# Optimization experiments

Hardware: AMD Instinct MI355X
Metric: run time of the kernel (lower is better)

The kernel has to match this reference:

```python
import jax, jax.numpy as jnp
import numpy as np

jax.config.update("jax_enable_x64", True)

P = 2013265921        # NTT-friendly prime (15 * 2^27 + 1), stand-in for BLS12-381 Fr
G_ROOT = 31           # primitive root of P
LOG_N = 21
N = 1 << LOG_N


def _bit_reverse_perm(n):
    logn = n.bit_length() - 1
    idx = np.arange(n, dtype=np.int64)
    rev = np.zeros(n, dtype=np.int64)
    for b in range(logn):
        rev = (rev << 1) | ((idx >> b) & 1)
    return rev


def _pow_arr(base, exps, mod):
    # vectorized modular exponentiation over numpy int64 exponents (host-side, trace-time)
    res = np.ones_like(exps)
    b = np.int64(base % mod)
    e = exps.copy()
    while e.max() > 0:
        res = np.where(e & 1, (res * b) % mod, res)
        b = (b * b) % mod
        e >>= 1
    return res


_REV = _bit_reverse_perm(N)


def intt(x):
    """Inverse NTT over Z_P, radix-2 DIT with bit-reversal. x: [N] int64 in [0,P)."""
    root = pow(G_ROOT, (P - 1) // N, P)
    iroot = pow(root, P - 2, P)
    x = x[_REV]
    length = 2
    while length <= N:
        half = length // 2
        wlen = pow(iroot, N // length, P)
        tw = jnp.asarray(_pow_arr(wlen, np.arange(half, dtype=np.int64), P))  # [half]
        x = x.reshape(-1, length)
        even, odd = x[:, :half], x[:, half:]
        t = (odd * tw) % P                       # products < 2^62, exact in int64
        x = jnp.concatenate([(even + t) % P, (even - t) % P], axis=1).reshape(-1)
        length *= 2
    n_inv = pow(N, P - 2, P)
    return (x * n_inv) % P


def compress4(a, b, c, d, z):
    """zkp.compress: a + z*b + z^2*c + z^3*d  (mod P). z is a Python int challenge."""
    z1 = z % P
    z2 = (z1 * z1) % P
    z3 = (z2 * z1) % P
    return (a + (b * z1) % P + (c * z2) % P + (d * z3) % P) % P


def commit(poly, bases):
    """KZG commitment proxy: MSM reduced to a scalar-weighted sum of SRS bases."""
    scal = poly.astype(jnp.float32) * np.float32(1.0 / P)  # normalize field elems
    return jnp.einsum('n,nc->c', scal, bases)              # [3]


def reference(w_l, w_r, w_o, w_4, table1, table2, table3, table4,
              q_lookup, powers_of_g, zeta):
    # Round 1: wire polynomials via INTT + commitments via MSM
    w_l_poly = intt(w_l)
    w_r_poly = intt(w_r)
    w_o_poly = intt(w_o)
    w_4_poly = intt(w_4)

    # Lookup: compress tables with zeta, build query table f, split sorted multiset
    t_comp = compress4(table1, table2, table3, table4, zeta)
    table_poly = intt(t_comp)
    w_comp = compress4(w_l, w_r, w_o, w_4, zeta)
    f_comp = jnp.where(q_lookup != 0, w_comp, t_comp)      # compute_query_table
    f_poly = intt(f_comp)

    s = jnp.sort(jnp.concatenate([t_comp, f_comp]))        # combine_split
    h_1, h_2 = s[0::2], s[1::2]
    h_1_poly = intt(h_1)
    h_2_poly = intt(h_2)

    polys = jnp.stack([w_l_poly, w_r_poly, w_o_poly, w_4_poly,
                       table_poly, f_poly, h_1_poly, h_2_poly])  # [8, N]
    commits = jnp.stack([commit(p, powers_of_g) for p in polys])  # [8, 3]
    return commits, polys


def setup_inputs() -> dict:
    key = jax.random.key(0)
    ks = jax.random.split(key, 11)
    fe = lambda k: jax.random.randint(k, (N,), 0, P, dtype=jnp.int64)
    return {
        'w_l': fe(ks[0]), 'w_r': fe(ks[1]), 'w_o': fe(ks[2]), 'w_4': fe(ks[3]),
        'table1': fe(ks[4]), 'table2': fe(ks[5]), 'table3': fe(ks[6]), 'table4': fe(ks[7]),
        'q_lookup': jax.random.randint(ks[8], (N,), 0, 2, dtype=jnp.int64),
        'powers_of_g': jax.random.normal(ks[9], (N, 3), dtype=jnp.float32),
        'zeta': 987654321,
    }
```

## Files before the change

kernel.cpp:

```cpp
#include <hip/hip_runtime.h>
#include <stdint.h>

#define PRIME 2013265921u
#define LOGN 21
#define NN (1u << LOGN)
#define REG 73728u

constexpr uint32_t cpow(uint64_t b, uint64_t e) {
    uint64_t r = 1;
    b %= PRIME;
    while (e) {
        if (e & 1ull) r = r * b % PRIME;
        b = b * b % PRIME;
        e >>= 1;
    }
    return (uint32_t)r;
}
constexpr uint32_t cpinv() {
    uint32_t inv = 1;
    for (int i = 0; i < 6; i++) inv *= 2u - PRIME * inv;
    return inv;
}
constexpr uint32_t NPRIME   = (uint32_t)(0u - cpinv());
constexpr uint32_t RMODP    = (uint32_t)((1ull << 32) % PRIME);
constexpr uint32_t ROOT     = cpow(31u, (PRIME - 1) / NN);
constexpr uint32_t IROOT    = cpow(ROOT, PRIME - 2);
constexpr uint32_t NINV     = cpow(NN, PRIME - 2);
constexpr uint32_t NINV_M   = (uint32_t)((((uint64_t)NINV) << 32) % PRIME);

__device__ __forceinline__ uint32_t addmod(uint32_t a, uint32_t b) {
    uint32_t s = a + b; return (s >= PRIME) ? s - PRIME : s;
}
__device__ __forceinline__ uint32_t submod(uint32_t a, uint32_t b) {
    return (a >= b) ? (a - b) : (a + PRIME - b);
}
__device__ __forceinline__ uint32_t mulmod(uint32_t a, uint32_t b) {
    return (uint32_t)(((uint64_t)a * (uint64_t)b) % PRIME);
}
__device__ __forceinline__ uint32_t montmul(uint32_t a, uint32_t b) {
    uint64_t t = (uint64_t)a * b;
    uint32_t m = (uint32_t)t * NPRIME;
    uint32_t u = (uint32_t)((t + (uint64_t)m * PRIME) >> 32);
    return (u >= PRIME) ? u - PRIME : u;
}
__device__ uint32_t powmod(uint32_t b, uint32_t e) {
    uint32_t r = 1u;
    while (e) {
        if (e & 1u) r = mulmod(r, b);
        b = mulmod(b, b);
        e >>= 1;
    }
    return r;
}
__device__ __forceinline__ uint32_t tomont(uint32_t x) {
    return (uint32_t)((((uint64_t)x) << 32) % PRIME);
}

__global__ void twiddle_all_kernel(uint32_t* __restrict__ WT1, uint32_t* __restrict__ ROWT,
                                   uint32_t* __restrict__ CW) {
    uint32_t i = blockIdx.x * blockDim.x + threadIdx.x;
    if (i < 4096) {
        if (i == 0) WT1[0] = RMODP;
        else {
            uint32_t s = 31u - __clz(i);
            uint32_t j = i ^ (1u << s);
            WT1[i] = tomont(powmod(IROOT, j << (20u - s)));
        }
    }
    if (i < 512) {
        if (i == 0) ROWT[0] = RMODP;
        else {
            uint32_t t = 31u - __clz(i);
            ROWT[i] = tomont(powmod(IROOT, (i - (1u << t)) << (20u - t)));
        }
    }
    if (i < 36864) {
        uint32_t s = i >> 12, j = i & 4095u;
        CW[i] = tomont(powmod(IROOT, j << (8u - s)));
    }
}

__global__ void init_cursor_kernel(unsigned int* __restrict__ ccursor) {
    if (threadIdx.x < 64) ccursor[threadIdx.x] = threadIdx.x * REG;
}

__global__ __launch_bounds__(256) void compress_scatter_kernel(
        const int* __restrict__ wl, const int* __restrict__ wr,
        const int* __restrict__ wo, const int* __restrict__ w4,
        const int* __restrict__ t1, const int* __restrict__ t2,
        const int* __restrict__ t3, const int* __restrict__ t4,
        const int* __restrict__ q,  const int* __restrict__ zp,
        uint32_t* __restrict__ tcomp, uint32_t* __restrict__ fcomp,
        unsigned int* __restrict__ ccursor, uint32_t* __restrict__ barr1) {
    __shared__ uint32_t grp[4096];
    __shared__ unsigned char grpb[4096];
    __shared__ unsigned int cnt[64], pref[64], curs[64], rbase[64];
    uint32_t tid = threadIdx.x;
    uint32_t i0 = blockIdx.x * 2048u + tid * 8u;
    if (tid < 64) cnt[tid] = 0;
    __syncthreads();

    uint32_t z1 = ((uint32_t)zp[0]) % PRIME;
    uint32_t z2 = mulmod(z1, z1);
    uint32_t z3 = mulmod(z2, z1);
    uint32_t tv[8], fv[8];
    #pragma unroll
    for (int h = 0; h < 2; h++) {
        uint32_t ib = i0 + (uint32_t)h * 4u;
        int4 a1 = *reinterpret_cast<const int4*>(&t1[ib]);
        int4 a2 = *reinterpret_cast<const int4*>(&t2[ib]);
        int4 a3 = *reinterpret_cast<const int4*>(&t3[ib]);
        int4 a4 = *reinterpret_cast<const int4*>(&t4[ib]);
        int4 b1 = *reinterpret_cast<const int4*>(&wl[ib]);
        int4 b2 = *reinterpret_cast<const int4*>(&wr[ib]);
        int4 b3 = *reinterpret_cast<const int4*>(&wo[ib]);
        int4 b4 = *reinterpret_cast<const int4*>(&w4[ib]);
        int4 qq = *reinterpret_cast<const int4*>(&q[ib]);
        int av1[4] = {a1.x, a1.y, a1.z, a1.w};
        int av2[4] = {a2.x, a2.y, a2.z, a2.w};
        int av3[4] = {a3.x, a3.y, a3.z, a3.w};
        int av4[4] = {a4.x, a4.y, a4.z, a4.w};
        int bv1[4] = {b1.x, b1.y, b1.z, b1.w};
        int bv2[4] = {b2.x, b2.y, b2.z, b2.w};
        int bv3[4] = {b3.x, b3.y, b3.z, b3.w};
        int bv4[4] = {b4.x, b4.y, b4.z, b4.w};
        int qv[4]  = {qq.x, qq.y, qq.z, qq.w};
        #pragma unroll
        for (int j = 0; j < 4; j++) {
            uint32_t t = addmod(addmod((uint32_t)av1[j], mulmod((uint32_t)av2[j], z1)),
                                addmod(mulmod((uint32_t)av3[j], z2), mulmod((uint32_t)av4[j], z3)));
            uint32_t w = addmod(addmod((uint32_t)bv1[j], mulmod((uint32_t)bv2[j], z1)),
                                addmod(mulmod((uint32_t)bv3[j], z2), mulmod((uint32_t)bv4[j], z3)));
            tv[h * 4 + j] = t;
            fv[h * 4 + j] = (qv[j] != 0) ? w : t;
        }
    }
    *reinterpret_cast<uint4*>(&tcomp[i0])     = make_uint4(tv[0], tv[1], tv[2], tv[3]);
    *reinterpret_cast<uint4*>(&tcomp[i0 + 4]) = make_uint4(tv[4], tv[5], tv[6], tv[7]);
    *reinterpret_cast<uint4*>(&fcomp[i0])     = make_uint4(fv[0], fv[1], fv[2], fv[3]);
    *reinterpret_cast<uint4*>(&fcomp[i0 + 4]) = make_uint4(fv[4], fv[5], fv[6], fv[7]);

    #pragma unroll
    for (int j = 0; j < 8; j++) {
        atomicAdd(&cnt[tv[j] >> 25], 1u);
        atomicAdd(&cnt[fv[j] >> 25], 1u);
    }
    __syncthreads();
    if (tid == 0) {
        unsigned int run = 0;
        for (int b = 0; b < 64; b++) { pref[b] = run; curs[b] = run; run += cnt[b]; }
    }
    __syncthreads();
    if (tid < 64 && cnt[tid]) rbase[tid] = atomicAdd(&ccursor[tid], cnt[tid]);
    #pragma unroll
    for (int j = 0; j < 8; j++) {
        uint32_t v = tv[j];
        uint32_t b = v >> 25;
        unsigned int p = atomicAdd(&curs[b], 1u);
        grp[p] = v; grpb[p] = (unsigned char)b;
    }
    #pragma unroll
    for (int j = 0; j < 8; j++) {
        uint32_t v = fv[j];
        uint32_t b = v >> 25;
        unsigned int p = atomicAdd(&curs[b], 1u);
        grp[p] = v; grpb[p] = (unsigned char)b;
    }
    __syncthreads();
    for (uint32_t l = tid; l < 4096; l += 256) {
        uint32_t b = grpb[l];
        barr1[rbase[b] + (l - pref[b])] = grp[l];
    }
}

#define NBUCK 8192

__global__ __launch_bounds__(256) void fine_hist_kernel(const uint32_t* __restrict__ barr1,
                                                        const unsigned int* __restrict__ ccursor,
                                                        unsigned int* __restrict__ hist) {
    __shared__ unsigned int cnt[128];
    uint32_t tid = threadIdx.x;
    uint32_t reg = blockIdx.y;
    if (tid < 128) cnt[tid] = 0;
    __syncthreads();
    uint32_t lo = reg * REG, hi = ccursor[reg];
    for (uint32_t i = lo + blockIdx.x * 256 + tid; i < hi; i += gridDim.x * 256)
        atomicAdd(&cnt[(barr1[i] >> 18) & 127u], 1u);
    __syncthreads();
    if (tid < 128 && cnt[tid]) atomicAdd(&hist[reg * 128 + tid], cnt[tid]);
}

__global__ void scan_kernel(const unsigned int* __restrict__ hist,
                            unsigned int* __restrict__ basearr, unsigned int* __restrict__ fcursor) {
    __shared__ unsigned int ls[256];
    int t = threadIdx.x;
    unsigned int local[32];
    unsigned int s = 0;
    for (int k = 0; k < 32; k++) { local[k] = hist[t * 32 + k]; s += local[k]; }
    ls[t] = s;
    __syncthreads();
    for (int off = 1; off < 256; off <<= 1) {
        unsigned int v = (t >= off) ? ls[t - off] : 0u;
        __syncthreads();
        ls[t] += v;
        __syncthreads();
    }
    unsigned int run = ls[t] - s;
    for (int k = 0; k < 32; k++) {
        basearr[t * 32 + k] = run;
        fcursor[t * 32 + k] = run;
        run += local[k];
    }
    if (t == 255) basearr[NBUCK] = run;
}

__global__ __launch_bounds__(256) void pass2_kernel(const uint32_t* __restrict__ barr1,
                                                    const unsigned int* __restrict__ ccursor,
                                                    unsigned int* __restrict__ fcursor,
                                                    uint32_t* __restrict__ barr2) {
    __shared__ uint32_t grp[4096];
    __shared__ unsigned char grpb[4096];
    __shared__ unsigned int cnt[128], pref[128], curs[128], rbase[128];
    uint32_t tid = threadIdx.x;
    uint32_t reg = blockIdx.y;
    uint32_t lo = reg * REG, hi = ccursor[reg];
    for (uint32_t start = lo + blockIdx.x * 4096; start < hi; start += gridDim.x * 4096) {
        uint32_t n = min(4096u, hi - start);
        if (tid < 128) cnt[tid] = 0;
        __syncthreads();
        for (uint32_t l = tid; l < n; l += 256)
            atomicAdd(&cnt[(barr1[start + l] >> 18) & 127u], 1u);
        __syncthreads();
        if (tid == 0) {
            unsigned int run = 0;
            for (int b = 0; b < 128; b++) { pref[b] = run; curs[b] = run; run += cnt[b]; }
        }
        __syncthreads();
        if (tid < 128 && cnt[tid]) rbase[tid] = atomicAdd(&fcursor[reg * 128 + tid], cnt[tid]);
        for (uint32_t l = tid; l < n; l += 256) {
            uint32_t v = barr1[start + l];
            uint32_t b = (v >> 18) & 127u;
            unsigned int p = atomicAdd(&curs[b], 1u);
            grp[p] = v; grpb[p] = (unsigned char)b;
        }
        __syncthreads();
        for (uint32_t l = tid; l < n; l += 256) {
            uint32_t b = grpb[l];
            barr2[rbase[b] + (l - pref[b])] = grp[l];
        }
        __syncthreads();
    }
}

__global__ __launch_bounds__(256) void bucket_sort_kernel(const uint32_t* __restrict__ barr,
                                                          const unsigned int* __restrict__ basearr,
                                                          uint32_t* __restrict__ h1, uint32_t* __restrict__ h2) {
    __shared__ uint32_t ord[4096];
    __shared__ unsigned int cnt[128], pref[128], curs[128];
    uint32_t b  = blockIdx.x;
    uint32_t lo = basearr[b], hi = basearr[b + 1];
    uint32_t n  = hi - lo;
    if (n == 0) return;
    if (n > 4096) n = 4096;
    uint32_t tid = threadIdx.x;
    if (tid < 128) cnt[tid] = 0;
    __syncthreads();
    for (uint32_t i = tid; i < n; i += 256)
        atomicAdd(&cnt[(barr[lo + i] >> 11) & 127u], 1u);
    __syncthreads();
    if (tid == 0) {
        unsigned int run = 0;
        for (int d = 0; d < 128; d++) { pref[d] = run; curs[d] = run; run += cnt[d]; }
    }
    __syncthreads();
    for (uint32_t i = tid; i < n; i += 256) {
        uint32_t v = barr[lo + i];
        uint32_t d = (v >> 11) & 127u;
        unsigned int p = atomicAdd(&curs[d], 1u);
        ord[p] = v;
    }
    __syncthreads();
    for (uint32_t p = tid; p < n; p += 256) {
        uint32_t v = ord[p];
        uint32_t d = (v >> 11) & 127u;
        uint32_t l0 = pref[d], l1 = l0 + cnt[d];
        uint32_t r = 0;
        for (uint32_t qq = l0; qq < l1; qq++) {
            uint32_t u = ord[qq];
            r += (u < v) || (u == v && qq < p);
        }
        uint32_t gp = lo + l0 + r;
        if (gp & 1) h2[gp >> 1] = v; else h1[gp >> 1] = v;
    }
}

struct SrcPtrs { const uint32_t* p[8]; };

__global__ void bitrev_kernel(SrcPtrs srcs, uint32_t* __restrict__ dst) {
    __shared__ uint32_t tile[64 * 65];
    uint32_t poly = blockIdx.y;
    const uint32_t* src = srcs.p[poly];
    uint32_t* out = dst + (size_t)poly * NN;
    uint32_t m  = blockIdx.x;
    uint32_t rm = __brev(m) >> 23;
    for (uint32_t l = threadIdx.x; l < 4096; l += blockDim.x) {
        uint32_t u = l >> 6, v = l & 63;
        tile[u * 65 + v] = src[(u << 15) | (rm << 6) | v];
    }
    __syncthreads();
    for (uint32_t l = threadIdx.x; l < 4096; l += blockDim.x) {
        uint32_t a = l >> 6, b = l & 63;
        uint32_t ra = __brev(a) >> 26, rb = __brev(b) >> 26;
        out[(a << 15) | (m << 6) | b] = tile[rb * 65 + ra];
    }
}

__device__ __forceinline__ uint32_t padi(uint32_t i) { return i + (i >> 5); }

__global__ __launch_bounds__(256) void ntt_phase1_kernel(uint32_t* __restrict__ polys,
                                                         const uint32_t* __restrict__ WT1) {
    __shared__ uint32_t wt[4096];
    __shared__ uint32_t sd[4224];
    uint32_t* x = polys + (size_t)blockIdx.y * NN + (size_t)blockIdx.x * 4096;
    #pragma unroll
    for (uint32_t m = 0; m < 4; m++) {
        uint32_t l = m * 1024 + threadIdx.x * 4;
        uint4 v = *reinterpret_cast<const uint4*>(&x[l]);
        uint4 w = *reinterpret_cast<const uint4*>(&WT1[l]);
        uint32_t p = padi(l);
        sd[p] = v.x; sd[p + 1] = v.y; sd[p + 2] = v.z; sd[p + 3] = v.w;
        *reinterpret_cast<uint4*>(&wt[l]) = w;
    }
    __syncthreads();
    #pragma unroll
    for (int t = 0; t < 6; t++) {
        uint32_t h = 1u << (2 * t);
        #pragma unroll
        for (uint32_t m = 0; m < 4; m++) {
            uint32_t q = threadIdx.x + (m << 8);
            uint32_t j = q & (h - 1);
            uint32_t grp = q >> (2 * t);
            uint32_t i0 = (grp << (2 * t + 2)) + j;
            uint32_t w1  = wt[h + j];
            uint32_t w2  = wt[2 * h + j];
            uint32_t w2j = wt[3 * h + j];
            uint32_t p0 = padi(i0), p1 = padi(i0 + h), p2 = padi(i0 + 2 * h), p3 = padi(i0 + 3 * h);
            uint32_t a0 = sd[p0], a1 = sd[p1], a2 = sd[p2], a3 = sd[p3];
            uint32_t t1 = montmul(w1, a1), t3 = montmul(w1, a3);
            uint32_t b0 = addmod(a0, t1), b1 = submod(a0, t1);
            uint32_t b2 = addmod(a2, t3), b3 = submod(a2, t3);
            uint32_t u2 = montmul(w2, b2), u3 = montmul(w2j, b3);
            sd[p0] = addmod(b0, u2);
            sd[p2] = submod(b0, u2);
            sd[p1] = addmod(b1, u3);
            sd[p3] = submod(b1, u3);
        }
        __syncthreads();
    }
    #pragma unroll
    for (uint32_t m = 0; m < 4; m++) {
        uint32_t l = m * 1024 + threadIdx.x * 4;
        uint32_t p = padi(l);
        uint4 v;
        v.x = montmul(sd[p], NINV_M);
        v.y = montmul(sd[p + 1], NINV_M);
        v.z = montmul(sd[p + 2], NINV_M);
        v.w = montmul(sd[p + 3], NINV_M);
        *reinterpret_cast<uint4*>(&x[l]) = v;
    }
}

__global__ __launch_bounds__(512) void ntt_phase2_kernel(uint32_t* __restrict__ polys,
                                                         const uint32_t* __restrict__ ROWT,
                                                         const uint32_t* __restrict__ CW,
                                                         const float* __restrict__ g,
                                                         double* __restrict__ partials) {
    __shared__ __align__(16) uint32_t sd[16384];
    uint32_t b = blockIdx.x;
    uint32_t xcd = b & 7u, k = b >> 3;
    uint32_t poly = k >> 4;
    uint32_t c0_idx = xcd * 16u + (k & 15u);
    uint32_t* x = polys + (size_t)poly * NN;
    uint32_t c0 = c0_idx * 32u;
    uint32_t tid = threadIdx.x;
    uint32_t c = tid & 31u;
    uint32_t rt = tid >> 5;
    uint32_t cg = tid & 7u;
    uint32_t r0 = tid >> 3;

    #pragma unroll
    for (uint32_t kk = 0; kk < 8; kk++) {
        uint32_t row = r0 + kk * 64;
        uint4 v = *reinterpret_cast<const uint4*>(&x[(row << 12) + c0 + 4 * cg]);
        *reinterpret_cast<uint4*>(&sd[row * 32 + 4 * cg]) = v;
    }
    uint32_t cw[9];
    #pragma unroll
    for (int s = 0; s < 9; s++) cw[s] = CW[s * 4096 + c0 + c];
    __syncthreads();

    #pragma unroll
    for (int s = 0; s < 8; s += 2) {
        uint32_t h = 1u << s;
        #pragma unroll
        for (uint32_t m = 0; m < 8; m++) {
            uint32_t u = (rt << 3) + m;
            uint32_t kk = u & (h - 1);
            uint32_t grp = u >> s;
            uint32_t r = (grp << (s + 2)) + kk;
            uint32_t w1  = montmul(ROWT[h + kk], cw[s]);
            uint32_t w2  = montmul(ROWT[2 * h + kk], cw[s + 1]);
            uint32_t w2j = montmul(ROWT[3 * h + kk], cw[s + 1]);
            uint32_t i0 = (r << 5) + c;
            uint32_t i1 = ((r + h) << 5) + c;
            uint32_t i2 = ((r + 2 * h) << 5) + c;
            uint32_t i3 = ((r + 3 * h) << 5) + c;
            uint32_t a0 = sd[i0], a1 = sd[i1], a2 = sd[i2], a3 = sd[i3];
            uint32_t t1 = montmul(w1, a1), t3 = montmul(w1, a3);
            uint32_t b0 = addmod(a0, t1), b1 = submod(a0, t1);
            uint32_t b2 = addmod(a2, t3), b3 = submod(a2, t3);
            uint32_t u2 = montmul(w2, b2), u3 = montmul(w2j, b3);
            sd[i0] = addmod(b0, u2);
            sd[i2] = submod(b0, u2);
            sd[i1] = addmod(b1, u3);
            sd[i3] = submod(b1, u3);
        }
        __syncthreads();
    }
    #pragma unroll
    for (uint32_t m = 0; m < 16; m++) {
        uint32_t kk = (rt << 4) + m;
        uint32_t w = montmul(ROWT[256 + kk], cw[8]);
        uint32_t i0 = (kk << 5) + c, i1 = ((kk + 256) << 5) + c;
        uint32_t u = sd[i0];
        uint32_t v = montmul(sd[i1], w);
        sd[i0] = addmod(u, v);
        sd[i1] = submod(u, v);
    }
    __syncthreads();

    float* xf = (float*)x;
    const float invp = (float)(1.0 / 2013265921.0);
    double a0 = 0.0, a1 = 0.0, a2 = 0.0;
    #pragma unroll
    for (uint32_t kk = 0; kk < 8; kk++) {
        uint32_t row = r0 + kk * 64;
        uint32_t idx0 = (row << 12) + c0 + 4 * cg;
        uint32_t base = row * 32 + 4 * cg;
        float f0 = (float)sd[base], f1 = (float)sd[base + 1];
        float f2 = (float)sd[base + 2], f3 = (float)sd[base + 3];
        float4 fv = make_float4(f0, f1, f2, f3);
        *reinterpret_cast<float4*>(&xf[idx0]) = fv;
        const float4* gp = reinterpret_cast<const float4*>(&g[(size_t)idx0 * 3]);
        float4 g0 = gp[0], g1 = gp[1], g2 = gp[2];
        float s0 = f0 * invp, s1 = f1 * invp, s2 = f2 * invp, s3 = f3 * invp;
        a0 += (double)(s0 * g0.x) + (double)(s1 * g0.w) + (double)(s2 * g1.z) + (double)(s3 * g2.y);
        a1 += (double)(s0 * g0.y) + (double)(s1 * g1.x) + (double)(s2 * g1.w) + (double)(s3 * g2.z);
        a2 += (double)(s0 * g0.z) + (double)(s1 * g1.y) + (double)(s2 * g2.x) + (double)(s3 * g2.w);
    }
    __syncthreads();
    double* red = (double*)sd;
    double v3[3] = {a0, a1, a2};
    #pragma unroll
    for (int kq = 0; kq < 3; kq++) {
        red[tid] = v3[kq];
        __syncthreads();
        for (int off = 256; off > 0; off >>= 1) {
            if (tid < off) red[tid] += red[tid + off];
            __syncthreads();
        }
        if (tid == 0) partials[((size_t)poly * 128 + c0_idx) * 3 + kq] = red[0];
        __syncthreads();
    }
}

__global__ void reduce_commits_kernel(const double* __restrict__ partials, float* __restrict__ outf) {
    __shared__ double red[256];
    int t = threadIdx.x;
    for (int k = 0; k < 24; k++) {
        int p = k / 3, cc = k % 3;
        red[t] = (t < 128) ? partials[((size_t)p * 128 + t) * 3 + cc] : 0.0;
        __syncthreads();
        for (int off = 128; off > 0; off >>= 1) {
            if (t < off) red[t] += red[t + off];
            __syncthreads();
        }
        if (t == 0) outf[k] = (float)red[0];
        __syncthreads();
    }
}

extern "C" void kernel_launch(void* const* d_in, const int* in_sizes, int n_in,
                              void* d_out, int out_size, void* d_ws, size_t ws_size,
                              hipStream_t stream) {
    const int* wl = (const int*)d_in[0];
    const int* wr = (const int*)d_in[1];
    const int* wo = (const int*)d_in[2];
    const int* w4 = (const int*)d_in[3];
    const int* t1 = (const int*)d_in[4];
    const int* t2 = (const int*)d_in[5];
    const int* t3 = (const int*)d_in[6];
    const int* t4 = (const int*)d_in[7];
    const int* q  = (const int*)d_in[8];
    const float* g = (const float*)d_in[9];
    const int* zp = (const int*)d_in[10];

    char* ws = (char*)d_ws;
    uint32_t* WT1  = (uint32_t*)(ws);
    uint32_t* ROWT = (uint32_t*)(ws + (64u  << 10));
    uint32_t* CW   = (uint32_t*)(ws + (128u << 10));
    uint32_t* tcomp  = (uint32_t*)(ws + (8ull  << 20));
    uint32_t* fcomp  = (uint32_t*)(ws + (16ull << 20));
    uint32_t* h1     = (uint32_t*)(ws + (24ull << 20));
    uint32_t* h2     = (uint32_t*)(ws + (32ull << 20));
    unsigned int* hist    = (unsigned int*)(ws + (40ull << 20));
    unsigned int* basearr = (unsigned int*)(ws + (40ull << 20) + (64u  << 10));
    unsigned int* fcursor = (unsigned int*)(ws + (40ull << 20) + (128u << 10));
    unsigned int* ccursor = (unsigned int*)(ws + (40ull << 20) + (232u << 10));
    double*       partials = (double*)    (ws + (40ull << 20) + (256u << 10));

    float* outf = (float*)d_out;
    uint32_t* outpolys = (uint32_t*)outf + 24;
    uint32_t* barr1 = (uint32_t*)outf + 1024;
    uint32_t* barr2 = (uint32_t*)outf + 1024 + (5u << 20);

    hipMemsetAsync(hist, 0, NBUCK * sizeof(unsigned int), stream);

    twiddle_all_kernel<<<144, 256, 0, stream>>>(WT1, ROWT, CW);
    init_cursor_kernel<<<1, 64, 0, stream>>>(ccursor);

    compress_scatter_kernel<<<1024, 256, 0, stream>>>(wl, wr, wo, w4, t1, t2, t3, t4, q, zp,
                                                      tcomp, fcomp, ccursor, barr1);
    fine_hist_kernel<<<dim3(16, 64), 256, 0, stream>>>(barr1, ccursor, hist);
    scan_kernel<<<1, 256, 0, stream>>>(hist, basearr, fcursor);
    pass2_kernel<<<dim3(16, 64), 256, 0, stream>>>(barr1, ccursor, fcursor, barr2);
    bucket_sort_kernel<<<NBUCK, 256, 0, stream>>>(barr2, basearr, h1, h2);

    SrcPtrs sp;
    sp.p[0] = (const uint32_t*)wl;
    sp.p[1] = (const uint32_t*)wr;
    sp.p[2] = (const uint32_t*)wo;
    sp.p[3] = (const uint32_t*)w4;
    sp.p[4] = tcomp;
    sp.p[5] = fcomp;
    sp.p[6] = h1;
    sp.p[7] = h2;
    bitrev_kernel<<<dim3(512, 8), 256, 0, stream>>>(sp, outpolys);
    ntt_phase1_kernel<<<dim3(512, 8), 256, 0, stream>>>(outpolys, WT1);
    ntt_phase2_kernel<<<1024, 512, 0, stream>>>(outpolys, ROWT, CW, g, partials);

    reduce_commits_kernel<<<1, 256, 0, stream>>>(partials, outf);
}
```

Measured before the change: 276.8 us.

## Replace fine histogram pass with fixed-capacity bucket regions in sort

```diff
diff --git a/kernel.cpp b/kernel.cpp
--- a/kernel.cpp
+++ b/kernel.cpp
@@ -5,6 +5,7 @@
 #define LOGN 21
 #define NN (1u << LOGN)
 #define REG 73728u
+#define FREG 768u
 
 constexpr uint32_t cpow(uint64_t b, uint64_t e) {
     uint64_t r = 1;
@@ -80,8 +81,11 @@
     }
 }
 
-__global__ void init_cursor_kernel(unsigned int* __restrict__ ccursor) {
-    if (threadIdx.x < 64) ccursor[threadIdx.x] = threadIdx.x * REG;
+__global__ void init_cursor_kernel(unsigned int* __restrict__ ccursor,
+                                   unsigned int* __restrict__ fcursor) {
+    uint32_t i = blockIdx.x * blockDim.x + threadIdx.x;
+    if (i < 8192) fcursor[i] = i * FREG;
+    if (i < 64) ccursor[i] = i * REG;
 }
 
 __global__ __launch_bounds__(256) void compress_scatter_kernel(
@@ -175,45 +179,6 @@
 
 #define NBUCK 8192
 
-__global__ __launch_bounds__(256) void fine_hist_kernel(const uint32_t* __restrict__ barr1,
-                                                        const unsigned int* __restrict__ ccursor,
-                                                        unsigned int* __restrict__ hist) {
-    __shared__ unsigned int cnt[128];
-    uint32_t tid = threadIdx.x;
-    uint32_t reg = blockIdx.y;
-    if (tid < 128) cnt[tid] = 0;
-    __syncthreads();
-    uint32_t lo = reg * REG, hi = ccursor[reg];
-    for (uint32_t i = lo + blockIdx.x * 256 + tid; i < hi; i += gridDim.x * 256)
-        atomicAdd(&cnt[(barr1[i] >> 18) & 127u], 1u);
-    __syncthreads();
-    if (tid < 128 && cnt[tid]) atomicAdd(&hist[reg * 128 + tid], cnt[tid]);
-}
-
-__global__ void scan_kernel(const unsigned int* __restrict__ hist,
-                            unsigned int* __restrict__ basearr, unsigned int* __restrict__ fcursor) {
-    __shared__ unsigned int ls[256];
-    int t = threadIdx.x;
-    unsigned int local[32];
-    unsigned int s = 0;
-    for (int k = 0; k < 32; k++) { local[k] = hist[t * 32 + k]; s += local[k]; }
-    ls[t] = s;
-    __syncthreads();
-    for (int off = 1; off < 256; off <<= 1) {
-        unsigned int v = (t >= off) ? ls[t - off] : 0u;
-        __syncthreads();
-        ls[t] += v;
-        __syncthreads();
-    }
-    unsigned int run = ls[t] - s;
-    for (int k = 0; k < 32; k++) {
-        basearr[t * 32 + k] = run;
-        fcursor[t * 32 + k] = run;
-        run += local[k];
-    }
-    if (t == 255) basearr[NBUCK] = run;
-}
-
 __global__ __launch_bounds__(256) void pass2_kernel(const uint32_t* __restrict__ barr1,
                                                     const unsigned int* __restrict__ ccursor,
                                                     unsigned int* __restrict__ fcursor,
@@ -252,16 +217,44 @@
     }
 }
 
+__global__ void scan_kernel(const unsigned int* __restrict__ fcursor,
+                            unsigned int* __restrict__ basearr) {
+    __shared__ unsigned int ls[256];
+    int t = threadIdx.x;
+    unsigned int local[32];
+    unsigned int s = 0;
+    for (int k = 0; k < 32; k++) {
+        uint32_t b = t * 32 + k;
+        local[k] = fcursor[b] - b * FREG;
+        s += local[k];
+    }
+    ls[t] = s;
+    __syncthreads();
+    for (int off = 1; off < 256; off <<= 1) {
+        unsigned int v = (t >= off) ? ls[t - off] : 0u;
+        __syncthreads();
+        ls[t] += v;
+        __syncthreads();
+    }
+    unsigned int run = ls[t] - s;
+    for (int k = 0; k < 32; k++) {
+        basearr[t * 32 + k] = run;
+        run += local[k];
+    }
+    if (t == 255) basearr[NBUCK] = run;
+}
+
 __global__ __launch_bounds__(256) void bucket_sort_kernel(const uint32_t* __restrict__ barr,
                                                           const unsigned int* __restrict__ basearr,
                                                           uint32_t* __restrict__ h1, uint32_t* __restrict__ h2) {
-    __shared__ uint32_t ord[4096];
+    __shared__ uint32_t ord[1024];
     __shared__ unsigned int cnt[128], pref[128], curs[128];
     uint32_t b  = blockIdx.x;
-    uint32_t lo = basearr[b], hi = basearr[b + 1];
-    uint32_t n  = hi - lo;
+    uint32_t obase = basearr[b];
+    uint32_t n = basearr[b + 1] - obase;
     if (n == 0) return;
-    if (n > 4096) n = 4096;
+    if (n > 1024) n = 1024;
+    uint32_t lo = b * FREG;
     uint32_t tid = threadIdx.x;
     if (tid < 128) cnt[tid] = 0;
     __syncthreads();
@@ -289,7 +282,7 @@
             uint32_t u = ord[qq];
             r += (u < v) || (u == v && qq < p);
         }
-        uint32_t gp = lo + l0 + r;
+        uint32_t gp = obase + l0 + r;
         if (gp & 1) h2[gp >> 1] = v; else h1[gp >> 1] = v;
     }
 }
@@ -513,7 +506,6 @@
     uint32_t* fcomp  = (uint32_t*)(ws + (16ull << 20));
     uint32_t* h1     = (uint32_t*)(ws + (24ull << 20));
     uint32_t* h2     = (uint32_t*)(ws + (32ull << 20));
-    unsigned int* hist    = (unsigned int*)(ws + (40ull << 20));
     unsigned int* basearr = (unsigned int*)(ws + (40ull << 20) + (64u  << 10));
     unsigned int* fcursor = (unsigned int*)(ws + (40ull << 20) + (128u << 10));
     unsigned int* ccursor = (unsigned int*)(ws + (40ull << 20) + (232u << 10));
@@ -524,16 +516,13 @@
     uint32_t* barr1 = (uint32_t*)outf + 1024;
     uint32_t* barr2 = (uint32_t*)outf + 1024 + (5u << 20);
 
-    hipMemsetAsync(hist, 0, NBUCK * sizeof(unsigned int), stream);
-
     twiddle_all_kernel<<<144, 256, 0, stream>>>(WT1, ROWT, CW);
-    init_cursor_kernel<<<1, 64, 0, stream>>>(ccursor);
+    init_cursor_kernel<<<32, 256, 0, stream>>>(ccursor, fcursor);
 
     compress_scatter_kernel<<<1024, 256, 0, stream>>>(wl, wr, wo, w4, t1, t2, t3, t4, q, zp,
                                                       tcomp, fcomp, ccursor, barr1);
-    fine_hist_kernel<<<dim3(16, 64), 256, 0, stream>>>(barr1, ccursor, hist);
-    scan_kernel<<<1, 256, 0, stream>>>(hist, basearr, fcursor);
     pass2_kernel<<<dim3(16, 64), 256, 0, stream>>>(barr1, ccursor, fcursor, barr2);
+    scan_kernel<<<1, 256, 0, stream>>>(fcursor, basearr);
     bucket_sort_kernel<<<NBUCK, 256, 0, stream>>>(barr2, basearr, h1, h2);
 
     SrcPtrs sp;
```

After: 265.2 us. 1.04x faster.
